# Optimization experiments

Hardware: AMD Instinct MI355X
Metric: run time of the kernel (lower is better)

The kernel has to match this reference:

```python
import jax, jax.numpy as jnp
import numpy as np

B, NQ, NK, E, H, F, L = 8, 300, 4096, 256, 8, 2048, 6
D = E // H
SCALE = D ** -0.5


def _ln(x, g, b):
    m = x.mean(-1, keepdims=True)
    v = ((x - m) ** 2).mean(-1, keepdims=True)
    return (x - m) / jnp.sqrt(v + 1e-5) * g + b


def _split_heads(x):
    b, n, _ = x.shape
    return x.reshape(b, n, H, D).transpose(0, 2, 1, 3)  # (B,H,N,D)


def _merge_heads(x):
    b, h, n, d = x.shape
    return x.transpose(0, 2, 1, 3).reshape(b, n, h * d)


def setup_inputs() -> dict:
    key = jax.random.key(0)
    c = [0]
    def nk():
        c[0] += 1
        return jax.random.fold_in(key, c[0])
    def p(shape):
        return jax.random.normal(nk(), shape, jnp.float32) * 0.02
    return {
        "tgt": jax.random.normal(nk(), (B, NQ, E), jnp.float32),
        "memory": jax.random.normal(nk(), (B, NK, E), jnp.float32),
        "geometry_mask": jax.random.randint(nk(), (B, NQ, NK), 0, 2).astype(bool),
        "sa_wqkv": p((L, 3 * E, E)), "sa_bqkv": p((L, 3 * E)),
        "sa_wo": p((L, E, E)), "sa_bo": p((L, E)),
        "ca_wq": p((L, E, E)), "ca_bq": p((L, E)),
        "ca_wk": p((L, E, E)), "ca_bk": p((L, E)),
        "ca_wv": p((L, E, E)), "ca_bv": p((L, E)),
        "ca_wo": p((L, E, E)), "ca_bo": p((L, E)),
        "f_w1": p((L, F, E)), "f_b1": p((L, F)),
        "f_w2": p((L, E, F)), "f_b2": p((L, E)),
        "ln1g": jnp.ones((L, E)), "ln1b": jnp.zeros((L, E)),
        "ln2g": jnp.ones((L, E)), "ln2b": jnp.zeros((L, E)),
        "ln3g": jnp.ones((L, E)), "ln3b": jnp.zeros((L, E)),
        "lnfg": jnp.ones((E,)), "lnfb": jnp.zeros((E,)),
    }


def _forward(tgt, memory, geometry_mask, params):
    mask4 = geometry_mask[:, None, :, :]  # (B,1,NQ,NK), broadcast over heads

    def step(t, p):
        (wqkv, bqkv, wo, bo, wq, bq, wk, bk, wv, bv, wco, bco,
         w1, b1, w2, b2, g1, be1, g2, be2, g3, be3) = p
        # --- self-attention (torch nn.MultiheadAttention, eval mode) ---
        qkv = t @ wqkv.T + bqkv
        q, k, v = jnp.split(qkv, 3, axis=-1)
        q, k, v = _split_heads(q), _split_heads(k), _split_heads(v)
        a = jax.nn.softmax(jnp.einsum('bhqd,bhkd->bhqk', q, k) * SCALE, axis=-1)
        sa = _merge_heads(jnp.einsum('bhqk,bhkd->bhqd', a, v)) @ wo.T + bo
        t = _ln(t + sa, g1, be1)
        # --- geometry-constrained cross-attention ---
        q = _split_heads(t @ wq.T + bq)
        k = _split_heads(memory @ wk.T + bk)
        v = _split_heads(memory @ wv.T + bv)
        s = jnp.einsum('bhqd,bhkd->bhqk', q, k) * SCALE
        s = jnp.where(mask4, s, -jnp.inf)  # masked_fill(~mask, -inf)
        a = jax.nn.softmax(s, axis=-1)
        ca = _merge_heads(jnp.einsum('bhqk,bhkd->bhqd', a, v)) @ wco.T + bco
        t = _ln(t + ca, g2, be2)
        # --- FFN ---
        f = jax.nn.relu(t @ w1.T + b1) @ w2.T + b2
        t = _ln(t + f, g3, be3)
        return t, None

    out, _ = jax.lax.scan(step, tgt, params)
    return out


def reference(tgt, memory, geometry_mask, sa_wqkv, sa_bqkv, sa_wo, sa_bo,
              ca_wq, ca_bq, ca_wk, ca_bk, ca_wv, ca_bv, ca_wo, ca_bo,
              f_w1, f_b1, f_w2, f_b2, ln1g, ln1b, ln2g, ln2b, ln3g, ln3b,
              lnfg, lnfb):
    params = (sa_wqkv, sa_bqkv, sa_wo, sa_bo, ca_wq, ca_bq, ca_wk, ca_bk,
              ca_wv, ca_bv, ca_wo, ca_bo, f_w1, f_b1, f_w2, f_b2,
              ln1g, ln1b, ln2g, ln2b, ln3g, ln3b)
    out = _forward(tgt, memory, geometry_mask, params)
    return _ln(out, lnfg, lnfb)
```

## Files before the change

### kernel.cpp

```cpp
#include <hip/hip_runtime.h>
#include <hip/hip_bf16.h>

constexpr int cB = 8, cNQ = 300, cNK = 4096, cE = 256, cH = 8, cD = 32, cF = 2048, cL = 6;
constexpr int MT = cB * cNQ;
constexpr int MM = cB * cNK;
constexpr int cQT = 10;
constexpr int cKS = 4;
constexpr float kScale = 0.17677669529663687f;

typedef __attribute__((ext_vector_type(8))) short short8_t;
typedef __attribute__((ext_vector_type(4))) short short4_t;
typedef __attribute__((ext_vector_type(4))) float float4_t;

__device__ inline short f2bf(float x) {
  __hip_bfloat16 h = __float2bfloat16(x);
  return __builtin_bit_cast(short, h);
}

__global__ void init_t(const float* __restrict__ in, float* __restrict__ t,
                       __hip_bfloat16* __restrict__ tb, int n) {
  int i = blockIdx.x * 256 + threadIdx.x;
  if (i < n) { float v = in[i]; t[i] = v; tb[i] = __float2bfloat16(v); }
}
__global__ void cast_f32_bf16(const float* __restrict__ in, __hip_bfloat16* __restrict__ out, int n) {
  int i = blockIdx.x * 256 + threadIdx.x;
  if (i < n) out[i] = __float2bfloat16(in[i]);
}

__global__ void pack_mask_T(const int* __restrict__ m, unsigned* __restrict__ mT) {
  int key = blockIdx.x * 256 + threadIdx.x;
  int qt = blockIdx.y, b = blockIdx.z;
  unsigned w = 0;
  for (int j = 0; j < 32; ++j) {
    int q = qt * 32 + j;
    unsigned bit = (q < cNQ) ? (unsigned)(m[((size_t)b * cNQ + q) * cNK + key] != 0) : 0u;
    w |= bit << j;
  }
  mT[((size_t)b * cQT + qt) * cNK + key] = w;
}

template<typename TA, typename TW, int EPI, int OMODE, typename TOUT>
__global__ __launch_bounds__(256) void gemm_mfma(const TA* __restrict__ A,
                                                 const TW* __restrict__ W,
                                                 const float* __restrict__ bias,
                                                 TOUT* __restrict__ C,
                                                 int M, int N, int K) {
  constexpr int LDSS = 72;
  __shared__ short As[64][LDSS];
  __shared__ short Ws[64][LDSS];
  int tid = threadIdx.x;
  int bm = blockIdx.x * 64, bn = blockIdx.y * 64;
  int lane = tid & 63, wave = tid >> 6;
  int m16 = lane & 15, quad = lane >> 4;
  int wm = (wave >> 1) * 32, wn = (wave & 1) * 32;

  int srow = tid >> 2;
  int kc = (tid & 3) * 16;
  bool aok = (bm + srow) < M;

  float4_t acc[2][2];
#pragma unroll
  for (int i = 0; i < 2; ++i)
#pragma unroll
    for (int j = 0; j < 2; ++j) acc[i][j] = (float4_t){0.f, 0.f, 0.f, 0.f};

  for (int k0 = 0; k0 < K; k0 += 64) {
    if constexpr (__hip_internal::is_same<TA, float>::value) {
      const float* src = A + (size_t)(bm + srow) * K + k0 + kc;
      short8_t p0, p1;
#pragma unroll
      for (int u = 0; u < 8; ++u) p0[u] = aok ? f2bf(src[u]) : (short)0;
#pragma unroll
      for (int u = 0; u < 8; ++u) p1[u] = aok ? f2bf(src[8 + u]) : (short)0;
      *(short8_t*)&As[srow][kc] = p0;
      *(short8_t*)&As[srow][kc + 8] = p1;
    } else {
      const TA* src = A + (size_t)(bm + srow) * K + k0 + kc;
      short8_t z = 0;
      *(short8_t*)&As[srow][kc] = aok ? *(const short8_t*)src : z;
      *(short8_t*)&As[srow][kc + 8] = aok ? *(const short8_t*)(src + 8) : z;
    }
    if constexpr (__hip_internal::is_same<TW, float>::value) {
      const float* src = W + (size_t)(bn + srow) * K + k0 + kc;
      short8_t p0, p1;
#pragma unroll
      for (int u = 0; u < 8; ++u) p0[u] = f2bf(src[u]);
#pragma unroll
      for (int u = 0; u < 8; ++u) p1[u] = f2bf(src[8 + u]);
      *(short8_t*)&Ws[srow][kc] = p0;
      *(short8_t*)&Ws[srow][kc + 8] = p1;
    } else {
      const TW* src = W + (size_t)(bn + srow) * K + k0 + kc;
      *(short8_t*)&Ws[srow][kc] = *(const short8_t*)src;
      *(short8_t*)&Ws[srow][kc + 8] = *(const short8_t*)(src + 8);
    }
    __syncthreads();
#pragma unroll
    for (int kk = 0; kk < 2; ++kk) {
      short8_t aF[2], bF[2];
#pragma unroll
      for (int i = 0; i < 2; ++i)
        aF[i] = *(const short8_t*)&As[wm + i * 16 + m16][kk * 32 + quad * 8];
#pragma unroll
      for (int j = 0; j < 2; ++j)
        bF[j] = *(const short8_t*)&Ws[wn + j * 16 + m16][kk * 32 + quad * 8];
#pragma unroll
      for (int i = 0; i < 2; ++i)
#pragma unroll
        for (int j = 0; j < 2; ++j)
          acc[i][j] = __builtin_amdgcn_mfma_f32_16x16x32_bf16(aF[i], bF[j], acc[i][j], 0, 0, 0);
    }
    __syncthreads();
  }

  if constexpr (OMODE == 2) {
#pragma unroll
    for (int i = 0; i < 2; ++i)
#pragma unroll
      for (int r = 0; r < 4; ++r) {
        int ml = wm + i * 16 + quad * 4 + r;
#pragma unroll
        for (int j = 0; j < 2; ++j) {
          int nl = wn + j * 16 + m16;
          Ws[nl][ml] = f2bf(acc[i][j][r] + bias[bn + nl]);
        }
      }
    __syncthreads();
    int nl = tid >> 2, mc = (tid & 3) * 16;
    if (bm + mc < M) {
      int n = bn + nl;
      __hip_bfloat16* dst = (__hip_bfloat16*)C +
          ((size_t)(n >> 5) * 32 + (n & 31)) * (size_t)M + bm + mc;
      *(short8_t*)dst = *(const short8_t*)&Ws[nl][mc];
      *(short8_t*)(dst + 8) = *(const short8_t*)&Ws[nl][mc + 8];
    }
  } else {
#pragma unroll
    for (int i = 0; i < 2; ++i) {
#pragma unroll
      for (int r = 0; r < 4; ++r) {
        int m = bm + wm + i * 16 + quad * 4 + r;
        if (m >= M) continue;
#pragma unroll
        for (int j = 0; j < 2; ++j) {
          int n = bn + wn + j * 16 + m16;
          float v = acc[i][j][r] + bias[n];
          if (EPI == 1) v = fmaxf(v, 0.f);
          if constexpr (OMODE == 1) {
            ((__hip_bfloat16*)C)[((size_t)(n >> 5) * M + m) * 32 + (n & 31)] = __float2bfloat16(v);
          } else if constexpr (__hip_internal::is_same<TOUT, float>::value) {
            C[(size_t)m * N + n] = v;
          } else {
            C[(size_t)m * N + n] = __float2bfloat16(v);
          }
        }
      }
    }
  }
}

template<typename TW, int EPI, int OMODE, typename TOUT>
__global__ __launch_bounds__(256) void gemm128(const __hip_bfloat16* __restrict__ A,
                                               const TW* __restrict__ W,
                                               const float* __restrict__ bias,
                                               TOUT* __restrict__ C,
                                               int M, int N, int K) {
  __shared__ short lds[2 * 128 * 72];
  auto As = (short(*)[72])lds;
  auto Ws = (short(*)[72])(lds + 128 * 72);
  int tid = threadIdx.x;
  int bm = blockIdx.x * 128, bn = blockIdx.y * 128;
  int lane = tid & 63, wave = tid >> 6;
  int n16 = lane & 15, quad = lane >> 4;
  int wm = (wave >> 1) * 64, wn = (wave & 1) * 64;
  int srow = tid >> 1, kc = (tid & 1) * 32;
  bool aok = (bm + srow) < M;

  float4_t acc[4][4];
#pragma unroll
  for (int i = 0; i < 4; ++i)
#pragma unroll
    for (int j = 0; j < 4; ++j) acc[i][j] = (float4_t){0.f, 0.f, 0.f, 0.f};

  for (int k0 = 0; k0 < K; k0 += 64) {
    {
      const __hip_bfloat16* src = A + (size_t)(bm + srow) * K + k0 + kc;
      short8_t z = 0;
#pragma unroll
      for (int u = 0; u < 4; ++u)
        *(short8_t*)&As[srow][kc + u * 8] = aok ? *(const short8_t*)(src + u * 8) : z;
    }
    if constexpr (__hip_internal::is_same<TW, float>::value) {
      const float* src = W + (size_t)(bn + srow) * K + k0 + kc;
#pragma unroll
      for (int u = 0; u < 4; ++u) {
        short8_t p;
#pragma unroll
        for (int v = 0; v < 8; ++v) p[v] = f2bf(src[u * 8 + v]);
        *(short8_t*)&Ws[srow][kc + u * 8] = p;
      }
    } else {
      const TW* src = W + (size_t)(bn + srow) * K + k0 + kc;
#pragma unroll
      for (int u = 0; u < 4; ++u)
        *(short8_t*)&Ws[srow][kc + u * 8] = *(const short8_t*)(src + u * 8);
    }
    __syncthreads();
#pragma unroll
    for (int kk = 0; kk < 2; ++kk) {
      short8_t aF[4], bF[4];
#pragma unroll
      for (int i = 0; i < 4; ++i)
        aF[i] = *(const short8_t*)&As[wm + i * 16 + n16][kk * 32 + quad * 8];
#pragma unroll
      for (int j = 0; j < 4; ++j)
        bF[j] = *(const short8_t*)&Ws[wn + j * 16 + n16][kk * 32 + quad * 8];
#pragma unroll
      for (int i = 0; i < 4; ++i)
#pragma unroll
        for (int j = 0; j < 4; ++j)
          acc[i][j] = __builtin_amdgcn_mfma_f32_16x16x32_bf16(aF[i], bF[j], acc[i][j], 0, 0, 0);
    }
    __syncthreads();
  }

  if constexpr (OMODE == 2) {
    auto TT = (short(*)[128])lds;
#pragma unroll
    for (int i = 0; i < 4; ++i)
#pragma unroll
      for (int r = 0; r < 4; ++r) {
        int ml = wm + i * 16 + quad * 4 + r;
#pragma unroll
        for (int j = 0; j < 4; ++j) {
          int nl = wn + j * 16 + n16;
          TT[nl][ml] = f2bf(acc[i][j][r] + bias[bn + nl]);
        }
      }
    __syncthreads();
    int nl = tid >> 1, mh = (tid & 1) * 64;
    int n = bn + nl;
    __hip_bfloat16* dst = (__hip_bfloat16*)C +
        ((size_t)(n >> 5) * 32 + (n & 31)) * (size_t)M + bm + mh;
#pragma unroll
    for (int ch = 0; ch < 8; ++ch) {
      if (bm + mh + ch * 8 < M)
        *(short8_t*)(dst + ch * 8) = *(const short8_t*)&TT[nl][mh + ch * 8];
    }
  } else {
#pragma unroll
    for (int i = 0; i < 4; ++i) {
#pragma unroll
      for (int r = 0; r < 4; ++r) {
        int m = bm + wm + i * 16 + quad * 4 + r;
        if (m >= M) continue;
#pragma unroll
        for (int j = 0; j < 4; ++j) {
          int n = bn + wn + j * 16 + n16;
          float v = acc[i][j][r] + bias[n];
          if (EPI == 1) v = fmaxf(v, 0.f);
          if constexpr (OMODE == 1) {
            ((__hip_bfloat16*)C)[((size_t)(n >> 5) * M + m) * 32 + (n & 31)] = __float2bfloat16(v);
          } else if constexpr (__hip_internal::is_same<TOUT, float>::value) {
            C[(size_t)m * N + n] = v;
          } else {
            C[(size_t)m * N + n] = __float2bfloat16(v);
          }
        }
      }
    }
  }
}

template<typename TQ, bool MASKED>
__global__ __launch_bounds__(64, 4) void attn_flash(
    const TQ* __restrict__ qb, size_t strQb, size_t strQh, int qRowStr,
    const __hip_bfloat16* __restrict__ kb, size_t strKb, size_t strKh, int kRowStr,
    const __hip_bfloat16* __restrict__ vt, size_t strVb, size_t strVh, size_t strVd,
    const unsigned* __restrict__ mT, size_t strMb,
    float* __restrict__ pO, size_t pStrO,
    float* __restrict__ pL, size_t pStrL,
    int nq, int nk, int kChunk) {
  int hb = blockIdx.x;
  int h = hb & 7, bz = hb >> 3;
  int qt = blockIdx.y, ks = blockIdx.z;
  int qbase = qt * 32;

  const TQ* q = qb + (size_t)bz * strQb + (size_t)h * strQh;
  const __hip_bfloat16* K = kb + (size_t)bz * strKb + (size_t)h * strKh;
  const __hip_bfloat16* V = vt + (size_t)bz * strVb + (size_t)h * strVh;
  const unsigned* mrow = MASKED ? (mT + (size_t)bz * strMb + (size_t)qt * cNK) : nullptr;

  int lane = threadIdx.x;
  int n16 = lane & 15, quad = lane >> 4;

  __shared__ short sP[32][40];

  short8_t qf[2];
#pragma unroll
  for (int qi = 0; qi < 2; ++qi) {
    qf[qi] = 0;
    int qr = qbase + qi * 16 + n16;
    if (qr < nq) {
      const TQ* qp = q + (size_t)qr * qRowStr + quad * 8;
      if constexpr (__hip_internal::is_same<TQ, float>::value) {
#pragma unroll
        for (int j = 0; j < 8; ++j) qf[qi][j] = f2bf(qp[j]);
      } else {
        qf[qi] = *(const short8_t*)qp;
      }
    }
  }
  short8_t ones;
#pragma unroll
  for (int j = 0; j < 8; ++j) ones[j] = f2bf(1.0f);

  float4_t accO[2][2], accL[2];
#pragma unroll
  for (int qi = 0; qi < 2; ++qi) {
    accL[qi] = (float4_t){0.f, 0.f, 0.f, 0.f};
#pragma unroll
    for (int di = 0; di < 2; ++di) accO[qi][di] = (float4_t){0.f, 0.f, 0.f, 0.f};
  }
  float4_t zero4 = {0.f, 0.f, 0.f, 0.f};

  int kbeg = ks * kChunk;
  int kend = kbeg + kChunk;
  if (kend > ((nk + 31) & ~31)) kend = (nk + 31) & ~31;
  for (int koff = kbeg; koff < kend; koff += 32) {
    int k0 = koff + 2 * n16;
    unsigned w0 = 0xFFFFFFFFu, w1 = 0xFFFFFFFFu;
    if (MASKED) {
      const unsigned* mp = mrow + k0;
      w0 = mp[0]; w1 = mp[1];
    }
    bool in0 = k0 < nk, in1 = (k0 + 1) < nk;
    short8_t kf0 = *(const short8_t*)(K + (size_t)k0 * kRowStr + quad * 8);
    short8_t kf1 = *(const short8_t*)(K + (size_t)(k0 + 1) * kRowStr + quad * 8);
    short8_t vf0 = *(const short8_t*)(V + (size_t)n16 * strVd + koff + quad * 8);
    short8_t vf1 = *(const short8_t*)(V + (size_t)(16 + n16) * strVd + koff + quad * 8);
    float4_t s00 = __builtin_amdgcn_mfma_f32_16x16x32_bf16(qf[0], kf0, zero4, 0, 0, 0);
    float4_t s01 = __builtin_amdgcn_mfma_f32_16x16x32_bf16(qf[0], kf1, zero4, 0, 0, 0);
    float4_t s10 = __builtin_amdgcn_mfma_f32_16x16x32_bf16(qf[1], kf0, zero4, 0, 0, 0);
    float4_t s11 = __builtin_amdgcn_mfma_f32_16x16x32_bf16(qf[1], kf1, zero4, 0, 0, 0);
#pragma unroll
    for (int qi = 0; qi < 2; ++qi) {
      const float4_t& sa = qi ? s10 : s00;
      const float4_t& sb = qi ? s11 : s01;
#pragma unroll
      for (int r = 0; r < 4; ++r) {
        int row = qi * 16 + quad * 4 + r;
        bool ok0 = in0, ok1 = in1;
        if (MASKED) {
          ok0 = ok0 && ((w0 >> row) & 1u);
          ok1 = ok1 && ((w1 >> row) & 1u);
        }
        float p0 = ok0 ? __expf(sa[r] * kScale) : 0.f;
        float p1 = ok1 ? __expf(sb[r] * kScale) : 0.f;
        unsigned pw = (unsigned)(unsigned short)f2bf(p0) |
                      ((unsigned)(unsigned short)f2bf(p1) << 16);
        *(unsigned*)&sP[row][2 * n16] = pw;
      }
    }
#pragma unroll
    for (int qi = 0; qi < 2; ++qi) {
      short8_t pf = *(const short8_t*)&sP[qi * 16 + n16][quad * 8];
      accO[qi][0] = __builtin_amdgcn_mfma_f32_16x16x32_bf16(pf, vf0, accO[qi][0], 0, 0, 0);
      accO[qi][1] = __builtin_amdgcn_mfma_f32_16x16x32_bf16(pf, vf1, accO[qi][1], 0, 0, 0);
      accL[qi]    = __builtin_amdgcn_mfma_f32_16x16x32_bf16(pf, ones, accL[qi], 0, 0, 0);
    }
  }

  size_t oBase = (size_t)ks * pStrO + (size_t)(bz * cNQ) * 256 + h * 32;
  size_t lBase = (size_t)ks * pStrL + (size_t)hb * 320;
#pragma unroll
  for (int qi = 0; qi < 2; ++qi) {
#pragma unroll
    for (int r = 0; r < 4; ++r) {
      int row = qi * 16 + quad * 4 + r;
      if (qbase + row >= nq) continue;
#pragma unroll
      for (int di = 0; di < 2; ++di)
        pO[oBase + (size_t)(qbase + row) * 256 + di * 16 + n16] = accO[qi][di][r];
      if (n16 == 0) pL[lBase + qbase + row] = accL[qi][r];
    }
  }
}

__global__ __launch_bounds__(64) void attn_merge(const float* __restrict__ pO,
                                                 const float* __restrict__ pL,
                                                 __hip_bfloat16* __restrict__ out) {
  int row = blockIdx.x;
  int lane = threadIdx.x;
  int c0 = lane * 4;
  int bz = row / cNQ, qq = row - bz * cNQ;
  int h = c0 >> 5;
  float l = 0.f;
#pragma unroll
  for (int ks = 0; ks < cKS; ++ks)
    l += pL[(size_t)ks * (64 * 320) + (size_t)(bz * 8 + h) * 320 + qq];
  float inv = 1.f / l;
  float o[4] = {0.f, 0.f, 0.f, 0.f};
#pragma unroll
  for (int ks = 0; ks < cKS; ++ks) {
    const float4_t v = *(const float4_t*)&pO[(size_t)ks * (MT * 256) + (size_t)row * 256 + c0];
#pragma unroll
    for (int u = 0; u < 4; ++u) o[u] += v[u];
  }
  short4_t res = {f2bf(o[0] * inv), f2bf(o[1] * inv), f2bf(o[2] * inv), f2bf(o[3] * inv)};
  *(short4_t*)&out[(size_t)row * 256 + c0] = res;
}

__global__ __launch_bounds__(64) void add_ln_k(float* __restrict__ t,
                                               __hip_bfloat16* __restrict__ tb,
                                               const float* __restrict__ delta,
                                               const float* __restrict__ g,
                                               const float* __restrict__ bb) {
  int r = blockIdx.x, lane = threadIdx.x;
  size_t base = (size_t)r * cE + lane * 4;
  float x[4];
  float s = 0.f;
#pragma unroll
  for (int i = 0; i < 4; ++i) { x[i] = t[base + i] + delta[base + i]; s += x[i]; }
  for (int off = 32; off; off >>= 1) s += __shfl_xor(s, off);
  float mean = s * (1.f / cE);
  float v = 0.f;
#pragma unroll
  for (int i = 0; i < 4; ++i) { float dd = x[i] - mean; v += dd * dd; }
  for (int off = 32; off; off >>= 1) v += __shfl_xor(v, off);
  float rstd = rsqrtf(v * (1.f / cE) + 1e-5f);
  float y[4];
#pragma unroll
  for (int i = 0; i < 4; ++i) {
    y[i] = (x[i] - mean) * rstd * g[lane * 4 + i] + bb[lane * 4 + i];
    t[base + i] = y[i];
  }
  short4_t pb = {f2bf(y[0]), f2bf(y[1]), f2bf(y[2]), f2bf(y[3])};
  *(short4_t*)&tb[base] = pb;
}

__global__ __launch_bounds__(64) void final_ln_k(const float* __restrict__ t,
                                                 const float* __restrict__ g,
                                                 const float* __restrict__ bb,
                                                 float* __restrict__ out) {
  int r = blockIdx.x, lane = threadIdx.x;
  size_t base = (size_t)r * cE + lane * 4;
  float x[4];
  float s = 0.f;
#pragma unroll
  for (int i = 0; i < 4; ++i) { x[i] = t[base + i]; s += x[i]; }
  for (int off = 32; off; off >>= 1) s += __shfl_xor(s, off);
  float mean = s * (1.f / cE);
  float v = 0.f;
#pragma unroll
  for (int i = 0; i < 4; ++i) { float dd = x[i] - mean; v += dd * dd; }
  for (int off = 32; off; off >>= 1) v += __shfl_xor(v, off);
  float rstd = rsqrtf(v * (1.f / cE) + 1e-5f);
#pragma unroll
  for (int i = 0; i < 4; ++i)
    out[base + i] = (x[i] - mean) * rstd * g[lane * 4 + i] + bb[lane * 4 + i];
}

struct Bufs {
  float *t, *s1, *s2, *pO, *pL;
  __hip_bfloat16 *tb, *big2, *vtq, *s1b, *s2b, *qbf, *ffnh, *kbuf, *vtb, *membf;
  unsigned* mTr;
  const float* memory;
  bool fullKV, precast;
};

template<typename TW>
static void run_layers(const TW* const* wt, const float* const* bs,
                       const float* ln1g, const float* ln1b,
                       const float* ln2g, const float* ln2b,
                       const float* ln3g, const float* ln3b,
                       Bufs B, hipStream_t stream) {
  const size_t pStrO = (size_t)MT * 256, pStrL = 64 * 320;
  for (int l = 0; l < cL; ++l) {
    const TW* wqkv = wt[0] + (size_t)l * 3 * cE * cE;  const float* bqkv = bs[0] + (size_t)l * 3 * cE;
    const TW* wo   = wt[1] + (size_t)l * cE * cE;      const float* bo   = bs[1] + (size_t)l * cE;
    const TW* wq   = wt[2] + (size_t)l * cE * cE;      const float* bq   = bs[2] + (size_t)l * cE;
    const TW* wk   = wt[3] + (size_t)l * cE * cE;      const float* bk   = bs[3] + (size_t)l * cE;
    const TW* wv   = wt[4] + (size_t)l * cE * cE;      const float* bv   = bs[4] + (size_t)l * cE;
    const TW* wco  = wt[5] + (size_t)l * cE * cE;      const float* bco  = bs[5] + (size_t)l * cE;
    const TW* w1   = wt[6] + (size_t)l * cF * cE;      const float* b1   = bs[6] + (size_t)l * cF;
    const TW* w2   = wt[7] + (size_t)l * cE * cF;      const float* b2   = bs[7] + (size_t)l * cE;

    gemm_mfma<__hip_bfloat16, TW, 0, 0, __hip_bfloat16><<<dim3(38, 8), 256, 0, stream>>>(
        B.tb, wqkv, bqkv, B.big2, MT, 512, cE);
    gemm_mfma<__hip_bfloat16, TW, 0, 2, __hip_bfloat16><<<dim3(38, 4), 256, 0, stream>>>(
        B.tb, wqkv + (size_t)512 * cE, bqkv + 512, B.vtq, MT, cE, cE);
    attn_flash<__hip_bfloat16, false><<<dim3(64, cQT, cKS), 64, 0, stream>>>(
        B.big2, (size_t)cNQ * 512, 32, 512,
        B.big2 + 256, (size_t)cNQ * 512, 32, 512,
        B.vtq, 300, (size_t)cD * MT, MT,
        nullptr, 0,
        B.pO, pStrO, B.pL, pStrL, cNQ, cNQ, 96);
    attn_merge<<<MT, 64, 0, stream>>>(B.pO, B.pL, B.s1b);
    gemm_mfma<__hip_bfloat16, TW, 0, 0, float><<<dim3(38, 4), 256, 0, stream>>>(
        B.s1b, wo, bo, B.s2, MT, cE, cE);
    add_ln_k<<<MT, 64, 0, stream>>>(B.t, B.tb, B.s2, ln1g + (size_t)l * cE, ln1b + (size_t)l * cE);
    gemm_mfma<__hip_bfloat16, TW, 0, 0, __hip_bfloat16><<<dim3(38, 4), 256, 0, stream>>>(
        B.tb, wq, bq, B.qbf, MT, cE, cE);
    if (B.fullKV && B.precast) {
      gemm128<TW, 0, 1, __hip_bfloat16><<<dim3(256, 2), 256, 0, stream>>>(
          B.membf, wk, bk, B.kbuf, MM, cE, cE);
      gemm128<TW, 0, 2, __hip_bfloat16><<<dim3(256, 2), 256, 0, stream>>>(
          B.membf, wv, bv, B.vtb, MM, cE, cE);
      attn_flash<__hip_bfloat16, true><<<dim3(64, cQT, cKS), 64, 0, stream>>>(
          B.qbf, (size_t)cNQ * cE, 32, cE,
          B.kbuf, (size_t)cNK * cD, (size_t)MM * cD, cD,
          B.vtb, (size_t)cNK, (size_t)cD * MM, MM,
          B.mTr, (size_t)cQT * cNK,
          B.pO, pStrO, B.pL, pStrL, cNQ, cNK, 1024);
      attn_merge<<<MT, 64, 0, stream>>>(B.pO, B.pL, B.s2b);
    } else {
      for (int b = 0; b < cB; ++b) {
        const float* memb = B.memory + (size_t)b * cNK * cE;
        gemm_mfma<float, TW, 0, 1, __hip_bfloat16><<<dim3(64, 4), 256, 0, stream>>>(
            memb, wk, bk, B.kbuf, cNK, cE, cE);
        gemm_mfma<float, TW, 0, 2, __hip_bfloat16><<<dim3(64, 4), 256, 0, stream>>>(
            memb, wv, bv, B.vtb, cNK, cE, cE);
        attn_flash<__hip_bfloat16, true><<<dim3(8, cQT, cKS), 64, 0, stream>>>(
            B.qbf + (size_t)b * cNQ * cE, 0, 32, cE,
            B.kbuf, 0, (size_t)cNK * cD, cD,
            B.vtb, 0, (size_t)cD * cNK, cNK,
            B.mTr + (size_t)b * cQT * cNK, 0,
            B.pO + (size_t)b * cNQ * 256, pStrO, B.pL + (size_t)b * 8 * 320, pStrL,
            cNQ, cNK, 1024);
      }
      attn_merge<<<MT, 64, 0, stream>>>(B.pO, B.pL, B.s2b);
    }
    gemm_mfma<__hip_bfloat16, TW, 0, 0, float><<<dim3(38, 4), 256, 0, stream>>>(
        B.s2b, wco, bco, B.s1, MT, cE, cE);
    add_ln_k<<<MT, 64, 0, stream>>>(B.t, B.tb, B.s1, ln2g + (size_t)l * cE, ln2b + (size_t)l * cE);
    gemm128<TW, 1, 0, __hip_bfloat16><<<dim3(19, 16), 256, 0, stream>>>(
        B.tb, w1, b1, B.ffnh, MT, cF, cE);
    gemm_mfma<__hip_bfloat16, TW, 0, 0, float><<<dim3(38, 4), 256, 0, stream>>>(
        B.ffnh, w2, b2, B.s1, MT, cE, cF);
    add_ln_k<<<MT, 64, 0, stream>>>(B.t, B.tb, B.s1, ln3g + (size_t)l * cE, ln3b + (size_t)l * cE);
  }
}

extern "C" void kernel_launch(void* const* d_in, const int* in_sizes, int n_in,
                              void* d_out, int out_size, void* d_ws, size_t ws_size,
                              hipStream_t stream) {
  (void)in_sizes; (void)n_in; (void)out_size;
  const float* tgt    = (const float*)d_in[0];
  const float* memory = (const float*)d_in[1];
  const int*   gmask  = (const int*)d_in[2];
  const float* w_in[8]  = {(const float*)d_in[3], (const float*)d_in[5], (const float*)d_in[7],
                           (const float*)d_in[9], (const float*)d_in[11], (const float*)d_in[13],
                           (const float*)d_in[15], (const float*)d_in[17]};
  const float* b_in[8]  = {(const float*)d_in[4], (const float*)d_in[6], (const float*)d_in[8],
                           (const float*)d_in[10], (const float*)d_in[12], (const float*)d_in[14],
                           (const float*)d_in[16], (const float*)d_in[18]};
  const size_t w_sz[8]  = {(size_t)cL*3*cE*cE, (size_t)cL*cE*cE, (size_t)cL*cE*cE,
                           (size_t)cL*cE*cE, (size_t)cL*cE*cE, (size_t)cL*cE*cE,
                           (size_t)cL*cF*cE, (size_t)cL*cE*cF};
  const float* ln1g = (const float*)d_in[19], *ln1b = (const float*)d_in[20];
  const float* ln2g = (const float*)d_in[21], *ln2b = (const float*)d_in[22];
  const float* ln3g = (const float*)d_in[23], *ln3b = (const float*)d_in[24];
  const float* lnfg = (const float*)d_in[25], *lnfb = (const float*)d_in[26];

  char* wp = (char*)d_ws;
  auto alloc = [&](size_t bytes) { void* p = wp; wp += (bytes + 255) & ~(size_t)255; return p; };

  Bufs B;
  B.memory = memory;
  B.t  = (float*)alloc((size_t)MT * cE * 4);
  B.s1 = (float*)alloc((size_t)MT * cE * 4);
  B.s2 = (float*)alloc((size_t)MT * cE * 4);
  B.tb = (__hip_bfloat16*)alloc((size_t)MT * cE * 2);
  B.big2 = (__hip_bfloat16*)alloc((size_t)MT * 512 * 2);
  B.vtq  = (__hip_bfloat16*)alloc((size_t)cH * cD * MT * 2);
  B.mTr = (unsigned*)alloc((size_t)cB * cQT * cNK * 4);
  B.pO = (float*)alloc((size_t)cKS * MT * 256 * 4);
  B.pL = (float*)alloc((size_t)cKS * 64 * 320 * 4);
  B.s1b = B.big2;
  B.s2b = B.big2 + (size_t)MT * 256;
  B.qbf = (__hip_bfloat16*)B.s1;
  B.ffnh = (__hip_bfloat16*)B.pO;

  size_t kvFull = (size_t)cH * MM * cD * 2;
  size_t used = (size_t)(wp - (char*)d_ws);
  B.fullKV = ws_size >= used + 2 * kvFull;
  if (B.fullKV) {
    B.kbuf = (__hip_bfloat16*)alloc(kvFull);
    B.vtb  = (__hip_bfloat16*)alloc(kvFull);
  } else {
    B.kbuf = (__hip_bfloat16*)alloc((size_t)cH * cNK * cD * 2);
    B.vtb  = (__hip_bfloat16*)alloc((size_t)cH * cNK * cD * 2);
  }
  size_t memBytes = (size_t)MM * cE * 2;
  used = (size_t)(wp - (char*)d_ws);
  B.precast = B.fullKV && (ws_size >= used + memBytes);
  B.membf = B.precast ? (__hip_bfloat16*)alloc(memBytes) : nullptr;

  size_t wbfTotal = 0;
  for (int i = 0; i < 8; ++i) wbfTotal += ((w_sz[i] * 2 + 255) & ~(size_t)255);
  used = (size_t)(wp - (char*)d_ws);
  bool wPre = ws_size >= used + wbfTotal;
  __hip_bfloat16* wbf[8] = {};
  if (wPre)
    for (int i = 0; i < 8; ++i) wbf[i] = (__hip_bfloat16*)alloc(w_sz[i] * 2);

  init_t<<<(MT * cE + 255) / 256, 256, 0, stream>>>(tgt, B.t, B.tb, MT * cE);
  pack_mask_T<<<dim3(cNK / 256, cQT, cB), 256, 0, stream>>>(gmask, B.mTr);
  if (B.precast)
    cast_f32_bf16<<<(MM * cE + 255) / 256, 256, 0, stream>>>(memory, B.membf, MM * cE);
  if (wPre)
    for (int i = 0; i < 8; ++i)
      cast_f32_bf16<<<(int)((w_sz[i] + 255) / 256), 256, 0, stream>>>(w_in[i], wbf[i], (int)w_sz[i]);

  if (wPre) {
    const __hip_bfloat16* wt[8];
    for (int i = 0; i < 8; ++i) wt[i] = wbf[i];
    run_layers<__hip_bfloat16>(wt, b_in, ln1g, ln1b, ln2g, ln2b, ln3g, ln3b, B, stream);
  } else {
    run_layers<float>(w_in, b_in, ln1g, ln1b, ln2g, ln2b, ln3g, ln3b, B, stream);
  }

  final_ln_k<<<MT, 64, 0, stream>>>(B.t, lnfg, lnfb, (float*)d_out);
}
```

Baseline: 1.264 ms.

## Split attention key loop across four waves with shared-memory reduction

The flash attention kernel now runs four waves per block. Each wave strides over a quarter of the key chunk, and the partial O and L accumulators are reduced through shared memory before one vectorised store. This raises parallelism per block and cuts the serial key-loop length per wave, at the cost of a block barrier, extra LDS traffic and more shared memory per block. MFMA sections are also wrapped in s_setprio to favour matrix issue.

```diff
diff --git a/kernel.cpp b/kernel.cpp
--- a/kernel.cpp
+++ b/kernel.cpp
@@ -273,7 +273,7 @@
 }
 
 template<typename TQ, bool MASKED>
-__global__ __launch_bounds__(64, 4) void attn_flash(
+__global__ __launch_bounds__(256) void attn_flash(
     const TQ* __restrict__ qb, size_t strQb, size_t strQh, int qRowStr,
     const __hip_bfloat16* __restrict__ kb, size_t strKb, size_t strKh, int kRowStr,
     const __hip_bfloat16* __restrict__ vt, size_t strVb, size_t strVh, size_t strVd,
@@ -291,10 +291,13 @@
   const __hip_bfloat16* V = vt + (size_t)bz * strVb + (size_t)h * strVh;
   const unsigned* mrow = MASKED ? (mT + (size_t)bz * strMb + (size_t)qt * cNK) : nullptr;
 
-  int lane = threadIdx.x;
+  int tid = threadIdx.x;
+  int lane = tid & 63, wave = tid >> 6;
   int n16 = lane & 15, quad = lane >> 4;
 
-  __shared__ short sP[32][40];
+  __shared__ float redO[4][32][33];
+  __shared__ float redL[4][32];
+  short* sPw = (short*)&redO[0][0][0] + wave * (32 * 40);
 
   short8_t qf[2];
 #pragma unroll
@@ -324,10 +327,10 @@
   }
   float4_t zero4 = {0.f, 0.f, 0.f, 0.f};
 
-  int kbeg = ks * kChunk;
-  int kend = kbeg + kChunk;
-  if (kend > ((nk + 31) & ~31)) kend = (nk + 31) & ~31;
-  for (int koff = kbeg; koff < kend; koff += 32) {
+  int kpad = (nk + 31) & ~31;
+  int kend = ks * kChunk + kChunk;
+  if (kend > kpad) kend = kpad;
+  for (int koff = ks * kChunk + wave * 32; koff < kend; koff += 128) {
     int k0 = koff + 2 * n16;
     unsigned w0 = 0xFFFFFFFFu, w1 = 0xFFFFFFFFu;
     if (MASKED) {
@@ -339,10 +342,12 @@
     short8_t kf1 = *(const short8_t*)(K + (size_t)(k0 + 1) * kRowStr + quad * 8);
     short8_t vf0 = *(const short8_t*)(V + (size_t)n16 * strVd + koff + quad * 8);
     short8_t vf1 = *(const short8_t*)(V + (size_t)(16 + n16) * strVd + koff + quad * 8);
+    __builtin_amdgcn_s_setprio(1);
     float4_t s00 = __builtin_amdgcn_mfma_f32_16x16x32_bf16(qf[0], kf0, zero4, 0, 0, 0);
     float4_t s01 = __builtin_amdgcn_mfma_f32_16x16x32_bf16(qf[0], kf1, zero4, 0, 0, 0);
     float4_t s10 = __builtin_amdgcn_mfma_f32_16x16x32_bf16(qf[1], kf0, zero4, 0, 0, 0);
     float4_t s11 = __builtin_amdgcn_mfma_f32_16x16x32_bf16(qf[1], kf1, zero4, 0, 0, 0);
+    __builtin_amdgcn_s_setprio(0);
 #pragma unroll
     for (int qi = 0; qi < 2; ++qi) {
       const float4_t& sa = qi ? s10 : s00;
@@ -359,31 +364,47 @@
         float p1 = ok1 ? __expf(sb[r] * kScale) : 0.f;
         unsigned pw = (unsigned)(unsigned short)f2bf(p0) |
                       ((unsigned)(unsigned short)f2bf(p1) << 16);
-        *(unsigned*)&sP[row][2 * n16] = pw;
-      }
-    }
+        *(unsigned*)&sPw[row * 40 + 2 * n16] = pw;
+      }
+    }
+    __builtin_amdgcn_s_setprio(1);
 #pragma unroll
     for (int qi = 0; qi < 2; ++qi) {
-      short8_t pf = *(const short8_t*)&sP[qi * 16 + n16][quad * 8];
+      short8_t pf = *(const short8_t*)&sPw[(qi * 16 + n16) * 40 + quad * 8];
       accO[qi][0] = __builtin_amdgcn_mfma_f32_16x16x32_bf16(pf, vf0, accO[qi][0], 0, 0, 0);
       accO[qi][1] = __builtin_amdgcn_mfma_f32_16x16x32_bf16(pf, vf1, accO[qi][1], 0, 0, 0);
       accL[qi]    = __builtin_amdgcn_mfma_f32_16x16x32_bf16(pf, ones, accL[qi], 0, 0, 0);
     }
-  }
-
-  size_t oBase = (size_t)ks * pStrO + (size_t)(bz * cNQ) * 256 + h * 32;
-  size_t lBase = (size_t)ks * pStrL + (size_t)hb * 320;
+    __builtin_amdgcn_s_setprio(0);
+  }
+
+  __syncthreads();
 #pragma unroll
   for (int qi = 0; qi < 2; ++qi) {
 #pragma unroll
     for (int r = 0; r < 4; ++r) {
       int row = qi * 16 + quad * 4 + r;
-      if (qbase + row >= nq) continue;
 #pragma unroll
       for (int di = 0; di < 2; ++di)
-        pO[oBase + (size_t)(qbase + row) * 256 + di * 16 + n16] = accO[qi][di][r];
-      if (n16 == 0) pL[lBase + qbase + row] = accL[qi][r];
-    }
+        redO[wave][row][di * 16 + n16] = accO[qi][di][r];
+      if (n16 == 0) redL[wave][row] = accL[qi][r];
+    }
+  }
+  __syncthreads();
+
+  size_t oBase = (size_t)ks * pStrO + (size_t)(bz * cNQ) * 256 + h * 32;
+  int row = tid >> 3, c0 = (tid & 7) * 4;
+  if (qbase + row < nq) {
+    float4_t o;
+#pragma unroll
+    for (int u = 0; u < 4; ++u)
+      o[u] = redO[0][row][c0 + u] + redO[1][row][c0 + u] +
+             redO[2][row][c0 + u] + redO[3][row][c0 + u];
+    *(float4_t*)&pO[oBase + (size_t)(qbase + row) * 256 + c0] = o;
+  }
+  if (tid < 32 && qbase + tid < nq) {
+    float l = redL[0][tid] + redL[1][tid] + redL[2][tid] + redL[3][tid];
+    pL[(size_t)ks * pStrL + (size_t)hb * 320 + qbase + tid] = l;
   }
 }
 
@@ -490,7 +511,7 @@
         B.tb, wqkv, bqkv, B.big2, MT, 512, cE);
     gemm_mfma<__hip_bfloat16, TW, 0, 2, __hip_bfloat16><<<dim3(38, 4), 256, 0, stream>>>(
         B.tb, wqkv + (size_t)512 * cE, bqkv + 512, B.vtq, MT, cE, cE);
-    attn_flash<__hip_bfloat16, false><<<dim3(64, cQT, cKS), 64, 0, stream>>>(
+    attn_flash<__hip_bfloat16, false><<<dim3(64, cQT, cKS), 256, 0, stream>>>(
         B.big2, (size_t)cNQ * 512, 32, 512,
         B.big2 + 256, (size_t)cNQ * 512, 32, 512,
         B.vtq, 300, (size_t)cD * MT, MT,
@@ -507,7 +528,7 @@
           B.membf, wk, bk, B.kbuf, MM, cE, cE);
       gemm128<TW, 0, 2, __hip_bfloat16><<<dim3(256, 2), 256, 0, stream>>>(
           B.membf, wv, bv, B.vtb, MM, cE, cE);
-      attn_flash<__hip_bfloat16, true><<<dim3(64, cQT, cKS), 64, 0, stream>>>(
+      attn_flash<__hip_bfloat16, true><<<dim3(64, cQT, cKS), 256, 0, stream>>>(
           B.qbf, (size_t)cNQ * cE, 32, cE,
           B.kbuf, (size_t)cNK * cD, (size_t)MM * cD, cD,
           B.vtb, (size_t)cNK, (size_t)cD * MM, MM,
@@ -521,7 +542,7 @@
             memb, wk, bk, B.kbuf, cNK, cE, cE);
         gemm_mfma<float, TW, 0, 2, __hip_bfloat16><<<dim3(64, 4), 256, 0, stream>>>(
             memb, wv, bv, B.vtb, cNK, cE, cE);
-        attn_flash<__hip_bfloat16, true><<<dim3(8, cQT, cKS), 64, 0, stream>>>(
+        attn_flash<__hip_bfloat16, true><<<dim3(8, cQT, cKS), 256, 0, stream>>>(
             B.qbf + (size_t)b * cNQ * cE, 0, 32, cE,
             B.kbuf, 0, (size_t)cNK * cD, cD,
             B.vtb, 0, (size_t)cD * cNK, cNK,
```

Result: no change. 1.282 ms (+1.4%).
